# Performance work log

Hardware: AMD Instinct MI355X
Metric: run time of the kernel (lower is better)

## Reference

```python
import jax, jax.numpy as jnp
import numpy as np

KH, KW, PAD, G = 3, 3, 1, 4  # kernel, padding, deformable groups


def _bilinear_gather(xg, py, px):
    """xg: [B,G,C,Hin,Win]; py,px: [B,G,K,H,W] sample coords.
    Returns [B,G,C,K,H,W] with zero padding outside the image (mmcv semantics)."""
    B, Gd, C, Hin, Win = xg.shape
    y0 = jnp.floor(py)
    x0 = jnp.floor(px)
    wy1 = py - y0
    wx1 = px - x0
    wy0 = 1.0 - wy1
    wx0 = 1.0 - wx1
    xf = xg.reshape(B, Gd, C, Hin * Win)

    def gather(yi, xi):
        valid = (yi >= 0) & (yi < Hin) & (xi >= 0) & (xi < Win)
        yc = jnp.clip(yi, 0, Hin - 1).astype(jnp.int32)
        xc = jnp.clip(xi, 0, Win - 1).astype(jnp.int32)
        lin = (yc * Win + xc).reshape(B, Gd, 1, -1)  # [B,G,1,K*H*W]
        v = jnp.take_along_axis(xf, lin, axis=3).reshape(B, Gd, C, *yi.shape[2:])
        return v * valid[:, :, None].astype(xg.dtype)

    return (gather(y0, x0) * (wy0 * wx0)[:, :, None]
            + gather(y0, x0 + 1) * (wy0 * wx1)[:, :, None]
            + gather(y0 + 1, x0) * (wy1 * wx0)[:, :, None]
            + gather(y0 + 1, x0 + 1) * (wy1 * wx1)[:, :, None])


def setup_inputs() -> dict:
    key = jax.random.key(0)
    k1, k2, k3, k4 = jax.random.split(key, 4)
    B, Cin, Cout, H, W = 8, 256, 256, 64, 64
    x = jax.random.normal(k1, (B, Cin, H, W), dtype=jnp.float32)
    shape = jax.random.normal(k2, (B, 4, H, W), dtype=jnp.float32)
    # conv_offset: 1x1 conv, 4 -> G*2*KH*KW = 72 channels, no bias
    w_offset = jax.random.normal(k3, (G * 2 * KH * KW, 4), dtype=jnp.float32) * 0.1
    # conv_adaption: deform conv weight, no bias
    w_deform = jax.random.normal(k4, (Cout, Cin, KH, KW), dtype=jnp.float32) * 0.01
    return {"x": x, "shape": shape, "w_offset": w_offset, "w_deform": w_deform}


def reference(x, shape, w_offset, w_deform):
    B, Cin, H, W = x.shape
    Cout = w_deform.shape[0]
    K = KH * KW
    # 1x1 offset-predicting conv on detached shape
    shape = jax.lax.stop_gradient(shape)
    offset = jnp.einsum('oc,bchw->bohw', w_offset, shape)  # [B, G*2*K, H, W]
    off = offset.reshape(B, G, K, 2, H, W)  # mmcv layout: (dy, dx) per tap
    dy, dx = off[:, :, :, 0], off[:, :, :, 1]  # [B,G,K,H,W]
    # base sampling grid for each kernel tap
    ky, kx = jnp.meshgrid(jnp.arange(KH), jnp.arange(KW), indexing='ij')
    ky = ky.reshape(-1)
    kx = kx.reshape(-1)
    base_y = (ky - PAD)[:, None, None] + jnp.arange(H)[None, :, None]  # [K,H,1]
    base_x = (kx - PAD)[:, None, None] + jnp.arange(W)[None, None, :]  # [K,1,W]
    py = base_y[None, None].astype(x.dtype) + dy  # [B,G,K,H,W]
    px = base_x[None, None].astype(x.dtype) + dx
    xg = x.reshape(B, G, Cin // G, H, W)
    sampled = _bilinear_gather(xg, py, px)  # [B,G,Cpg,K,H,W]
    wr = w_deform.reshape(Cout, G, Cin // G, K)
    out = jnp.einsum('ogck,bgckhw->bohw', wr, sampled)
    return jax.nn.relu(out)
```

## Files before the change

kernel.cpp:

```cpp
#include <hip/hip_runtime.h>
#include <hip/hip_bf16.h>


#define Bn   8
#define CIN  256
#define COUT 256
#define Hn   64
#define Wn   64
#define Gn   4
#define Kn   9
#define CPG  64
#define GK   36

typedef float    f32x4 __attribute__((ext_vector_type(4)));
typedef _Float16 f16x2 __attribute__((ext_vector_type(2)));
typedef _Float16 f16x8 __attribute__((ext_vector_type(8)));

#define SWPAD 1156
#define HWT   32
__global__ void fa_prep(const float* __restrict__ x, const float* __restrict__ w,
                        _Float16* __restrict__ xt, _Float16* __restrict__ wfrag) {
    const int bid = blockIdx.x, t = threadIdx.x;
    __shared__ __align__(16) _Float16 spool[16 * SWPAD];
    if (bid < 1024) {
        _Float16* sT = spool;
        const int b = bid >> 7, tile = bid & 127;
        const int hw0 = tile * HWT;
        const int s = t >> 3, hwq = t & 7;
#pragma unroll
        for (int it = 0; it < 8; it++) {
            int c = it * 32 + s;
            float4 v = *(const float4*)(x + (((size_t)(b * CIN + c)) << 12) + hw0 + hwq * 4);
            const float* vf = (const float*)&v;
#pragma unroll
            for (int j = 0; j < 4; j++) {
                int hw = hwq * 4 + j;
                sT[hw * 256 + (c ^ (hwq << 3))] = (_Float16)vf[j];
            }
        }
        __syncthreads();
        const int cg = t & 31, hwr = t >> 5;
#pragma unroll
        for (int it = 0; it < 4; it++) {
            int hw = it * 8 + hwr;
            int q = hw >> 2;
            f16x8 v = *(const f16x8*)&sT[hw * 256 + ((cg ^ q) << 3)];
            *(f16x8*)&xt[(((size_t)b << 12) + hw0 + hw) * 256 + cg * 8] = v;
        }
    } else {
        _Float16* sw = spool;
        const int mt = (bid - 1024) >> 1, gh = (bid - 1024) & 1;
        const int o0 = mt * 16, g0 = gh * 2;
        const int r = t >> 4, tr = t & 15;
        const float* wp = w + (size_t)(o0 + r) * (CIN * Kn) + g0 * (CPG * Kn);
#pragma unroll
        for (int it = 0; it < 18; it++) {
            int off = it * 64 + tr * 4;
            float4 v = *(const float4*)(wp + off);
            _Float16* d = &sw[r * SWPAD + off];
            d[0] = (_Float16)v.x; d[1] = (_Float16)v.y;
            d[2] = (_Float16)v.z; d[3] = (_Float16)v.w;
        }
        __syncthreads();
#pragma unroll
        for (int it = 0; it < 9; it++) {
            int chunk = it * 256 + t;
            int lane = chunk & 63, ks = (chunk >> 6) & 1, gkl = chunk >> 7;
            int gl = gkl / Kn, k = gkl - gl * Kn;
            int gk = g0 * Kn + gkl;
            int ol = lane & 15;
            int cbase = ks * 32 + (lane >> 4) * 8;
            f16x8 v;
#pragma unroll
            for (int j = 0; j < 8; j++)
                v[j] = sw[ol * SWPAD + (gl * CPG + cbase + j) * Kn + k];
            *(f16x8*)&wfrag[(((size_t)gk * 16 + mt) * 2 + ks) * 512 + lane * 8] = v;
        }
    }
}

__global__ __launch_bounds__(512, 4)
void fa_main(const _Float16* __restrict__ xt, const float* __restrict__ shp,
             const float* __restrict__ w_off, const _Float16* __restrict__ wfrag,
             float* __restrict__ out) {
    const int blk = blockIdx.x;
    const int xcd = blk & 7, slot = blk >> 3;
    const int bp = xcd >> 1;
    const int h = (slot >> 1) * 2 + (xcd & 1);
    const int wh = slot & 1;
    const int w0 = wh * 32;
    const int t = threadIdx.x;
    const int wid = t >> 6, lane = t & 63;
    const int col = lane & 15, quad = lane >> 4;
    const int cg = t & 7, nl = (t >> 3) & 63;

    __shared__ int  s_meta_a[GK * 64];
    __shared__ __align__(8) int2 s_meta_w[GK * 64];
    __shared__ __align__(16) _Float16 sB[2][64 * 64];
    __shared__ float s_shp[2 * 4 * 32];
    __shared__ float s_woff[GK * 8];

    if (t < 256) {
        int bb = t >> 7, c = (t >> 5) & 3, wl = t & 31;
        s_shp[t] = shp[(((bp * 2 + bb) * 4 + c) << 12) + h * Wn + w0 + wl];
    }
    for (int u = t; u < GK * 8; u += 512) s_woff[u] = w_off[u];
    __syncthreads();

    for (int i = t; i < GK * 64; i += 512) {
        int gk = i >> 6, n = i & 63;
        int bb = n >> 5, wl = n & 31;
        int g = gk / Kn, k = gk - g * Kn;
        int ky = k / 3, kx = k - ky * 3;
        float dy = 0.f, dx = 0.f;
#pragma unroll
        for (int c = 0; c < 4; c++) {
            float sv = s_shp[(bb * 4 + c) * 32 + wl];
            dy = fmaf(s_woff[gk * 8 + c],     sv, dy);
            dx = fmaf(s_woff[gk * 8 + 4 + c], sv, dx);
        }
        float py = (float)(h + ky - 1) + dy;
        float px = (float)(w0 + wl + kx - 1) + dx;
        float y0 = floorf(py), x0 = floorf(px);
        float fy = py - y0, fx = px - x0;
        int iy = (int)y0, ix = (int)x0;
        bool y0v = (unsigned)iy       < (unsigned)Hn;
        bool y1v = (unsigned)(iy + 1) < (unsigned)Hn;
        bool x0v = (unsigned)ix       < (unsigned)Wn;
        bool x1v = (unsigned)(ix + 1) < (unsigned)Wn;
        int yc0 = min(max(iy, 0), Hn - 1), yc1 = min(max(iy + 1, 0), Hn - 1);
        int xc0 = min(max(ix, 0), Wn - 1), xc1 = min(max(ix + 1, 0), Wn - 1);
        int l00 = yc0 * Wn + xc0;
        int dx1 = xc1 - xc0, dy1 = yc1 - yc0;
        float wy1 = fy, wy0 = 1.f - fy, wx1 = fx, wx0 = 1.f - fx;
        float w00 = (y0v && x0v) ? wy0 * wx0 : 0.f;
        float w01 = (y0v && x1v) ? wy0 * wx1 : 0.f;
        float w10 = (y1v && x0v) ? wy1 * wx0 : 0.f;
        float w11 = (y1v && x1v) ? wy1 * wx1 : 0.f;
        f16x2 p0, p1;
        p0.x = (_Float16)w00; p0.y = (_Float16)w01;
        p1.x = (_Float16)w10; p1.y = (_Float16)w11;
        s_meta_a[i] = l00 | (dx1 << 12) | (dy1 << 13);
        s_meta_w[i] = make_int2(__builtin_bit_cast(int, p0),
                                __builtin_bit_cast(int, p1));
    }

    f16x8 c4[4];
    int2  amv;
    const unsigned nBase = ((unsigned)(bp * 2 + (nl >> 5)) << 20) + (unsigned)cg * 8u;

    auto issue = [&](int gk) {
        int aw = s_meta_a[gk * 64 + nl];
        amv = s_meta_w[gk * 64 + nl];
        unsigned g = (unsigned)gk / (unsigned)Kn;
        const _Float16* p = xt + nBase + g * 64u;
        unsigned a00 = ((unsigned)aw & 0xFFFu) << 8;
        unsigned dxo = ((unsigned)aw & 0x1000u) >> 4;
        unsigned dyo = ((unsigned)aw & 0x2000u) << 1;
        c4[0] = *(const f16x8*)(p + a00);
        c4[1] = *(const f16x8*)(p + a00 + dxo);
        c4[2] = *(const f16x8*)(p + a00 + dyo);
        c4[3] = *(const f16x8*)(p + a00 + (dxo + dyo));
    };
    auto commit = [&](int buf) {
        f16x2 wv0 = __builtin_bit_cast(f16x2, amv.x);
        f16x2 wv1 = __builtin_bit_cast(f16x2, amv.y);
        f16x2 w00 = __builtin_shufflevector(wv0, wv0, 0, 0);
        f16x2 w01 = __builtin_shufflevector(wv0, wv0, 1, 1);
        f16x2 w10 = __builtin_shufflevector(wv1, wv1, 0, 0);
        f16x2 w11 = __builtin_shufflevector(wv1, wv1, 1, 1);
        const f16x2* a0p = (const f16x2*)&c4[0];
        const f16x2* a1p = (const f16x2*)&c4[1];
        const f16x2* a2p = (const f16x2*)&c4[2];
        const f16x2* a3p = (const f16x2*)&c4[3];
        f16x8 r;
        f16x2* rp = (f16x2*)&r;
#pragma unroll
        for (int p = 0; p < 4; p++) {
            f16x2 rv = w00 * a0p[p] + w01 * a1p[p]
                     + w10 * a2p[p] + w11 * a3p[p];
            rp[p] = rv;
        }
        *(f16x8*)&sB[buf][(nl * 8 + (cg ^ (nl & 7))) * 8] = r;
    };

    f32x4 acc[2][4];
#pragma unroll
    for (int mt = 0; mt < 2; mt++)
#pragma unroll
        for (int nt = 0; nt < 4; nt++) acc[mt][nt] = (f32x4){0.f, 0.f, 0.f, 0.f};

    __syncthreads();

    issue(0);
    commit(0);
    issue(1);
    __syncthreads();

    for (int gk = 0; gk < GK; gk++) {
        const int buf = gk & 1;
        const _Float16* wbase = wfrag + (((size_t)gk * 16 + wid * 2) * 2) * 512;
        f16x8 af[2][2];
#pragma unroll
        for (int ks = 0; ks < 2; ks++)
#pragma unroll
            for (int mt = 0; mt < 2; mt++)
                af[ks][mt] = *(const f16x8*)(wbase + ((size_t)(mt * 2 + ks) * 64 + lane) * 8);
        f16x8 bfv[2][4];
#pragma unroll
        for (int ks = 0; ks < 2; ks++)
#pragma unroll
            for (int nt = 0; nt < 4; nt++) {
                int n = nt * 16 + col;
                int cq8 = ks * 4 + quad;
                bfv[ks][nt] = *(const f16x8*)&sB[buf][(n * 8 + (cq8 ^ (n & 7))) * 8];
            }
        if (gk + 1 < GK) commit(buf ^ 1);
        if (gk + 2 < GK) issue(gk + 2);
#pragma unroll
        for (int ks = 0; ks < 2; ks++)
#pragma unroll
            for (int mt = 0; mt < 2; mt++)
#pragma unroll
                for (int nt = 0; nt < 4; nt++)
                    acc[mt][nt] = __builtin_amdgcn_mfma_f32_16x16x32_f16(
                        af[ks][mt], bfv[ks][nt], acc[mt][nt], 0, 0, 0);
        asm volatile("s_waitcnt lgkmcnt(0)" ::: "memory");
        __builtin_amdgcn_s_barrier();
    }

#pragma unroll
    for (int mt = 0; mt < 2; mt++)
#pragma unroll
        for (int r = 0; r < 4; r++) {
            int o = wid * 32 + mt * 16 + quad * 4 + r;
#pragma unroll
            for (int nt = 0; nt < 4; nt++) {
                int n = nt * 16 + col;
                int b = bp * 2 + (n >> 5);
                int w = w0 + (n & 31);
                out[(((size_t)(b * COUT + o)) << 12) + h * Wn + w] =
                    fmaxf(acc[mt][nt][r], 0.f);
            }
        }
}

extern "C" void kernel_launch(void* const* d_in, const int* in_sizes, int n_in,
                              void* d_out, int out_size, void* d_ws, size_t ws_size,
                              hipStream_t stream) {
    const float* x     = (const float*)d_in[0];
    const float* shp   = (const float*)d_in[1];
    const float* w_off = (const float*)d_in[2];
    const float* w_def = (const float*)d_in[3];
    float* out = (float*)d_out;
    _Float16* wfrag = (_Float16*)d_ws;
    _Float16* xt    = (_Float16*)((char*)d_ws + (2u << 20));

    fa_prep<<<1024 + 32, 256, 0, stream>>>(x, w_def, xt, wfrag);
    fa_main<<<512, 512, 0, stream>>>(xt, shp, w_off, wfrag, out);
}
```

Before: 140.5 us.

## Process two gk taps per barrier with deeper gather prefetch pipeline

The main loop now handles two kernel-tap/group slices per iteration, with two register sets of gathered corners and a doubled shared B buffer. Gathers run two steps further ahead, and block-wide barriers drop from one per tap to one per pair. This should hide more global-gather latency and cut sync overhead. The cost is more registers and twice the LDS for sB, which could reduce occupancy under the 512x4 launch bound.

```diff
diff --git a/kernel.cpp b/kernel.cpp
--- a/kernel.cpp
+++ b/kernel.cpp
@@ -78,6 +78,69 @@
         }
     }
 }
+
+
+#define ISSUE(C4, AMV, gk) do {                                              \
+    int aw_ = s_meta_a[(gk) * 64 + nl];                                      \
+    AMV = s_meta_w[(gk) * 64 + nl];                                          \
+    unsigned g_ = (unsigned)(gk) / (unsigned)Kn;                             \
+    const _Float16* p_ = xt + nBase + g_ * 64u;                              \
+    unsigned a00_ = ((unsigned)aw_ & 0xFFFu) << 8;                           \
+    unsigned dxo_ = ((unsigned)aw_ & 0x1000u) >> 4;                          \
+    unsigned dyo_ = ((unsigned)aw_ & 0x2000u) << 1;                          \
+    C4[0] = *(const f16x8*)(p_ + a00_);                                      \
+    C4[1] = *(const f16x8*)(p_ + a00_ + dxo_);                               \
+    C4[2] = *(const f16x8*)(p_ + a00_ + dyo_);                               \
+    C4[3] = *(const f16x8*)(p_ + a00_ + (dxo_ + dyo_));                      \
+} while (0)
+
+#define COMMIT(C4, AMV, BUF, SUB) do {                                       \
+    f16x2 wv0_ = __builtin_bit_cast(f16x2, AMV.x);                           \
+    f16x2 wv1_ = __builtin_bit_cast(f16x2, AMV.y);                           \
+    f16x2 w00_ = __builtin_shufflevector(wv0_, wv0_, 0, 0);                  \
+    f16x2 w01_ = __builtin_shufflevector(wv0_, wv0_, 1, 1);                  \
+    f16x2 w10_ = __builtin_shufflevector(wv1_, wv1_, 0, 0);                  \
+    f16x2 w11_ = __builtin_shufflevector(wv1_, wv1_, 1, 1);                  \
+    const f16x2* a0p_ = (const f16x2*)&C4[0];                                \
+    const f16x2* a1p_ = (const f16x2*)&C4[1];                                \
+    const f16x2* a2p_ = (const f16x2*)&C4[2];                                \
+    const f16x2* a3p_ = (const f16x2*)&C4[3];                                \
+    f16x8 r_;                                                                \
+    f16x2* rp_ = (f16x2*)&r_;                                                \
+    _Pragma("unroll")                                                        \
+    for (int p = 0; p < 4; p++)                                              \
+        rp_[p] = w00_ * a0p_[p] + w01_ * a1p_[p]                             \
+               + w10_ * a2p_[p] + w11_ * a3p_[p];                            \
+    *(f16x8*)&sB[BUF][SUB][(nl * 8 + (cg ^ (nl & 7))) * 8] = r_;             \
+} while (0)
+
+#define HALF(GKI, RB, SUB, PIPE) do {                                        \
+    const _Float16* wbase_ = wfrag + (((size_t)(GKI) * 16 + wid * 2) * 2) * 512; \
+    f16x8 af_[2][2];                                                         \
+    _Pragma("unroll")                                                        \
+    for (int ks = 0; ks < 2; ks++)                                           \
+        _Pragma("unroll")                                                    \
+        for (int mt = 0; mt < 2; mt++)                                       \
+            af_[ks][mt] = *(const f16x8*)(wbase_ + ((size_t)(mt * 2 + ks) * 64 + lane) * 8); \
+    f16x8 bfv_[2][4];                                                        \
+    _Pragma("unroll")                                                        \
+    for (int ks = 0; ks < 2; ks++)                                           \
+        _Pragma("unroll")                                                    \
+        for (int nt = 0; nt < 4; nt++) {                                     \
+            int n = nt * 16 + col;                                           \
+            int cq8 = ks * 4 + quad;                                         \
+            bfv_[ks][nt] = *(const f16x8*)&sB[RB][SUB][(n * 8 + (cq8 ^ (n & 7))) * 8]; \
+        }                                                                    \
+    PIPE                                                                     \
+    _Pragma("unroll")                                                        \
+    for (int ks = 0; ks < 2; ks++)                                           \
+        _Pragma("unroll")                                                    \
+        for (int mt = 0; mt < 2; mt++)                                       \
+            _Pragma("unroll")                                                 \
+            for (int nt = 0; nt < 4; nt++)                                   \
+                acc[mt][nt] = __builtin_amdgcn_mfma_f32_16x16x32_f16(        \
+                    af_[ks][mt], bfv_[ks][nt], acc[mt][nt], 0, 0, 0);        \
+} while (0)
 
 __global__ __launch_bounds__(512, 4)
 void fa_main(const _Float16* __restrict__ xt, const float* __restrict__ shp,
@@ -96,7 +159,7 @@
 
     __shared__ int  s_meta_a[GK * 64];
     __shared__ __align__(8) int2 s_meta_w[GK * 64];
-    __shared__ __align__(16) _Float16 sB[2][64 * 64];
+    __shared__ __align__(16) _Float16 sB[2][2][64 * 64];
     __shared__ float s_shp[2 * 4 * 32];
     __shared__ float s_woff[GK * 8];
 
@@ -145,45 +208,10 @@
                                 __builtin_bit_cast(int, p1));
     }
 
-    f16x8 c4[4];
-    int2  amv;
+    f16x8 c4a[4], c4b[4];
+    int2  amva, amvb;
     const unsigned nBase = ((unsigned)(bp * 2 + (nl >> 5)) << 20) + (unsigned)cg * 8u;
 
-    auto issue = [&](int gk) {
-        int aw = s_meta_a[gk * 64 + nl];
-        amv = s_meta_w[gk * 64 + nl];
-        unsigned g = (unsigned)gk / (unsigned)Kn;
-        const _Float16* p = xt + nBase + g * 64u;
-        unsigned a00 = ((unsigned)aw & 0xFFFu) << 8;
-        unsigned dxo = ((unsigned)aw & 0x1000u) >> 4;
-        unsigned dyo = ((unsigned)aw & 0x2000u) << 1;
-        c4[0] = *(const f16x8*)(p + a00);
-        c4[1] = *(const f16x8*)(p + a00 + dxo);
-        c4[2] = *(const f16x8*)(p + a00 + dyo);
-        c4[3] = *(const f16x8*)(p + a00 + (dxo + dyo));
-    };
-    auto commit = [&](int buf) {
-        f16x2 wv0 = __builtin_bit_cast(f16x2, amv.x);
-        f16x2 wv1 = __builtin_bit_cast(f16x2, amv.y);
-        f16x2 w00 = __builtin_shufflevector(wv0, wv0, 0, 0);
-        f16x2 w01 = __builtin_shufflevector(wv0, wv0, 1, 1);
-        f16x2 w10 = __builtin_shufflevector(wv1, wv1, 0, 0);
-        f16x2 w11 = __builtin_shufflevector(wv1, wv1, 1, 1);
-        const f16x2* a0p = (const f16x2*)&c4[0];
-        const f16x2* a1p = (const f16x2*)&c4[1];
-        const f16x2* a2p = (const f16x2*)&c4[2];
-        const f16x2* a3p = (const f16x2*)&c4[3];
-        f16x8 r;
-        f16x2* rp = (f16x2*)&r;
-#pragma unroll
-        for (int p = 0; p < 4; p++) {
-            f16x2 rv = w00 * a0p[p] + w01 * a1p[p]
-                     + w10 * a2p[p] + w11 * a3p[p];
-            rp[p] = rv;
-        }
-        *(f16x8*)&sB[buf][(nl * 8 + (cg ^ (nl & 7))) * 8] = r;
-    };
-
     f32x4 acc[2][4];
 #pragma unroll
     for (int mt = 0; mt < 2; mt++)
@@ -192,39 +220,23 @@
 
     __syncthreads();
 
-    issue(0);
-    commit(0);
-    issue(1);
+    ISSUE(c4a, amva, 0);
+    ISSUE(c4b, amvb, 1);
+    COMMIT(c4a, amva, 0, 0);
+    ISSUE(c4a, amva, 2);
+    COMMIT(c4b, amvb, 0, 1);
+    ISSUE(c4b, amvb, 3);
     __syncthreads();
 
-    for (int gk = 0; gk < GK; gk++) {
-        const int buf = gk & 1;
-        const _Float16* wbase = wfrag + (((size_t)gk * 16 + wid * 2) * 2) * 512;
-        f16x8 af[2][2];
-#pragma unroll
-        for (int ks = 0; ks < 2; ks++)
-#pragma unroll
-            for (int mt = 0; mt < 2; mt++)
-                af[ks][mt] = *(const f16x8*)(wbase + ((size_t)(mt * 2 + ks) * 64 + lane) * 8);
-        f16x8 bfv[2][4];
-#pragma unroll
-        for (int ks = 0; ks < 2; ks++)
-#pragma unroll
-            for (int nt = 0; nt < 4; nt++) {
-                int n = nt * 16 + col;
-                int cq8 = ks * 4 + quad;
-                bfv[ks][nt] = *(const f16x8*)&sB[buf][(n * 8 + (cq8 ^ (n & 7))) * 8];
-            }
-        if (gk + 1 < GK) commit(buf ^ 1);
-        if (gk + 2 < GK) issue(gk + 2);
-#pragma unroll
-        for (int ks = 0; ks < 2; ks++)
-#pragma unroll
-            for (int mt = 0; mt < 2; mt++)
-#pragma unroll
-                for (int nt = 0; nt < 4; nt++)
-                    acc[mt][nt] = __builtin_amdgcn_mfma_f32_16x16x32_f16(
-                        af[ks][mt], bfv[ks][nt], acc[mt][nt], 0, 0, 0);
+    for (int P = 0; P < GK / 2; P++) {
+        const int rb = P & 1, wb = rb ^ 1;
+        const int g0 = 2 * P;
+        HALF(g0, rb, 0,
+             if (g0 + 2 < GK) COMMIT(c4a, amva, wb, 0);
+             if (g0 + 4 < GK) ISSUE(c4a, amva, g0 + 4); );
+        HALF(g0 + 1, rb, 1,
+             if (g0 + 3 < GK) COMMIT(c4b, amvb, wb, 1);
+             if (g0 + 5 < GK) ISSUE(c4b, amvb, g0 + 5); );
         asm volatile("s_waitcnt lgkmcnt(0)" ::: "memory");
         __builtin_amdgcn_s_barrier();
     }
```

New measurement: 138.1 us (median of 2 runs). No clear change (-1.7%).
